# Kernel optimization log

Measured on AMD Instinct MI355X. Metric: run time of the kernel, lower is better.

## Reference

```python
import jax, jax.numpy as jnp
import numpy as np

DIM = 1024
HEADS = 16
DIM_HEAD = DIM // HEADS
SCALE = DIM_HEAD ** -0.5
LN_EPS = 1e-5


def setup_inputs() -> dict:
    key = jax.random.key(0)
    ks = jax.random.split(key, 7)
    b, n = 4, 2048
    x = jax.random.normal(ks[0], (b, n, DIM), dtype=jnp.float32)
    pos = jax.random.normal(ks[1], (b, n, DIM), dtype=jnp.float32)
    # params (torch Linear init-like scale)
    w_qkv = jax.random.normal(ks[2], (DIM, 3 * DIM), dtype=jnp.float32) * (DIM ** -0.5)
    w_out = jax.random.normal(ks[3], (DIM, DIM), dtype=jnp.float32) * (DIM ** -0.5)
    b_out = jax.random.normal(ks[4], (DIM,), dtype=jnp.float32) * 0.01
    ln_gamma = jnp.ones((DIM,), dtype=jnp.float32)
    ln_beta = jnp.zeros((DIM,), dtype=jnp.float32)
    return {"x": x, "pos": pos, "w_qkv": w_qkv, "w_out": w_out,
            "b_out": b_out, "ln_gamma": ln_gamma, "ln_beta": ln_beta}


def _layer_norm(x, gamma, beta):
    mu = jnp.mean(x, axis=-1, keepdims=True)
    var = jnp.mean(jnp.square(x - mu), axis=-1, keepdims=True)
    return (x - mu) * jax.lax.rsqrt(var + LN_EPS) * gamma + beta


def reference(x, pos, w_qkv, w_out, b_out, ln_gamma, ln_beta):
    b, n, _ = x.shape
    xn = _layer_norm(x, ln_gamma, ln_beta)
    qkv = xn @ w_qkv                                    # [b, n, 3*dim]
    q, k, v = jnp.split(qkv, 3, axis=-1)
    # [b, n, dim] -> [b, h, n, d]
    to_heads = lambda t: t.reshape(b, n, HEADS, DIM_HEAD).transpose(0, 2, 1, 3)
    q, k, v = to_heads(q), to_heads(k), to_heads(v)
    scores = jnp.einsum('bhid,bhjd->bhij', q, k) * SCALE  # [b, h, n, n]
    attn = jax.nn.softmax(scores, axis=-1)
    out = jnp.einsum('bhij,bhjd->bhid', attn, v)          # [b, h, n, d]
    out = out.transpose(0, 2, 1, 3).reshape(b, n, DIM)    # [b, n, dim]
    return (out + pos) @ w_out + b_out
```

## Files before the change

kernel.cpp:

```cpp
#include <hip/hip_runtime.h>
#include <math.h>
#include <stdint.h>

#define TOKENS 8192
#define DIM 1024
#define N3 3072
#define NSEQ 2048
#define NH 16
#define DH 64

typedef __attribute__((ext_vector_type(8))) __bf16 bf16x8;
typedef __attribute__((ext_vector_type(4))) float f32x4;
typedef __attribute__((ext_vector_type(16))) float f32x16;
typedef __attribute__((ext_vector_type(4))) short short4v;

__device__ __forceinline__ unsigned cvt2bf(float a, float b) {
    unsigned r;
    asm("v_cvt_pk_bf16_f32 %0, %1, %2" : "=v"(r) : "v"(a), "v"(b));
    return r;
}
__device__ __forceinline__ unsigned short f2bf(float f) {
    unsigned r;
    asm("v_cvt_pk_bf16_f32 %0, %1, %1" : "=v"(r) : "v"(f));
    return (unsigned short)r;
}
__device__ __forceinline__ float exp2_raw(float x) {
    float r;
    asm("v_exp_f32 %0, %1" : "=v"(r) : "v"(x));
    return r;
}
__device__ __forceinline__ float max3f(float a, float b, float c) {
    float d;
    asm("v_max3_f32 %0, %1, %2, %3" : "=v"(d) : "v"(a), "v"(b), "v"(c));
    return d;
}

__device__ __forceinline__ void glds16(const void* g, void* l) {
    __builtin_amdgcn_global_load_lds((__attribute__((address_space(1))) void*)(void*)g,
                                     (__attribute__((address_space(3))) void*)l, 16, 0, 0);
}

__global__ __launch_bounds__(256) void transpose_to_bf16(
    const float* __restrict__ in, unsigned short* __restrict__ out, int R, int C) {
    __shared__ float tile[64][65];
    int n0 = blockIdx.x * 64, k0 = blockIdx.y * 64;
    int t = threadIdx.x;
#pragma unroll
    for (int i = 0; i < 16; i++) {
        int idx = i * 256 + t;
        int r = idx >> 6, c = idx & 63;
        tile[r][c] = in[(size_t)(k0 + r) * C + n0 + c];
    }
    __syncthreads();
#pragma unroll
    for (int i = 0; i < 16; i++) {
        int idx = i * 256 + t;
        int r = idx >> 6, c = idx & 63;
        out[(size_t)(n0 + r) * R + k0 + c] = f2bf(tile[c][r]);
    }
}

__global__ __launch_bounds__(256) void ln_kernel(
    const float* __restrict__ x, const float* __restrict__ gamma,
    const float* __restrict__ beta, unsigned short* __restrict__ xn) {
    int row = blockIdx.x;
    int t = threadIdx.x;
    const float4 v = ((const float4*)(x + (size_t)row * DIM))[t];
    float s = v.x + v.y + v.z + v.w;
    float sq = v.x * v.x + v.y * v.y + v.z * v.z + v.w * v.w;
#pragma unroll
    for (int m = 1; m < 64; m <<= 1) {
        s += __shfl_xor(s, m);
        sq += __shfl_xor(sq, m);
    }
    __shared__ float ws[4], wq[4];
    int w = t >> 6, lane = t & 63;
    if (lane == 0) { ws[w] = s; wq[w] = sq; }
    __syncthreads();
    s = ws[0] + ws[1] + ws[2] + ws[3];
    sq = wq[0] + wq[1] + wq[2] + wq[3];
    float mu = s * (1.0f / DIM);
    float var = sq * (1.0f / DIM) - mu * mu;
    float rstd = rsqrtf(var + 1e-5f);
    const float4 g = ((const float4*)gamma)[t];
    const float4 bb = ((const float4*)beta)[t];
    uint2 o;
    o.x = cvt2bf((v.x - mu) * rstd * g.x + bb.x, (v.y - mu) * rstd * g.y + bb.y);
    o.y = cvt2bf((v.z - mu) * rstd * g.z + bb.z, (v.w - mu) * rstd * g.w + bb.w);
    *(uint2*)(xn + (size_t)row * DIM + t * 4) = o;
}

__device__ __forceinline__ void xcd_swizzle(int& bx, int& by) {
    int nwgx = gridDim.x;
    int nwg = nwgx * gridDim.y;
    int wg = by * nwgx + bx;
    int cpx = nwg >> 3;
    int swz = (wg & 7) * cpx + (wg >> 3);
    bx = swz % nwgx;
    by = swz / nwgx;
}

__device__ __forceinline__ void gemm_stage(
    const unsigned short* __restrict__ A, const unsigned short* __restrict__ Bt, int K,
    int brow, int bcol, int k0, char* Abuf, char* Bbuf, int w, int srow, int scol) {
#pragma unroll
    for (int i = 0; i < 2; i++) {
        int c = i * 4 + w;
        glds16(A + (size_t)(brow + 16 * c + srow) * K + k0 + scol, Abuf + c * 1024);
        glds16(Bt + (size_t)(bcol + 16 * c + srow) * K + k0 + scol, Bbuf + c * 1024);
    }
}

__device__ __forceinline__ void gemm_core(
    const unsigned short* __restrict__ A, const unsigned short* __restrict__ Bt, int K,
    int brow, int bcol, char* As, char* Bs, f32x4 acc[4][4]) {
    int t = threadIdx.x, w = t >> 6, lane = t & 63;
    int wr = w >> 1, wc = w & 1;
    int srow = lane >> 2, scol = (lane & 3) * 8;
    char* a0 = As; char* a1 = As + 8192; char* a2 = As + 16384;
    char* b0 = Bs; char* b1 = Bs + 8192; char* b2 = Bs + 16384;
    gemm_stage(A, Bt, K, brow, bcol, 0, a0, b0, w, srow, scol);
    gemm_stage(A, Bt, K, brow, bcol, 32, a1, b1, w, srow, scol);
    int NT = K >> 5;
    for (int kt = 0; kt < NT; kt++) {
        asm volatile("s_waitcnt vmcnt(4)" ::: "memory");
        __builtin_amdgcn_s_barrier();
        int kn = kt + 2; if (kn >= NT) kn -= NT;
        gemm_stage(A, Bt, K, brow, bcol, kn << 5, a2, b2, w, srow, scol);
        bf16x8 a[4], b[4];
#pragma unroll
        for (int i = 0; i < 4; i++) {
            a[i] = *(const bf16x8*)(a0 + (wr * 64 + i * 16 + (lane & 15)) * 64 + (lane >> 4) * 16);
            b[i] = *(const bf16x8*)(b0 + (wc * 64 + i * 16 + (lane & 15)) * 64 + (lane >> 4) * 16);
        }
        __builtin_amdgcn_s_setprio(1);
#pragma unroll
        for (int i = 0; i < 4; i++)
#pragma unroll
            for (int j = 0; j < 4; j++)
                acc[i][j] = __builtin_amdgcn_mfma_f32_16x16x32_bf16(a[i], b[j], acc[i][j], 0, 0, 0);
        __builtin_amdgcn_s_setprio(0);
        char* tp;
        tp = a0; a0 = a1; a1 = a2; a2 = tp;
        tp = b0; b0 = b1; b1 = b2; b2 = tp;
    }
}

#define QSCALE_LOG2E 0.18033688011112042f

__global__ __launch_bounds__(256) void gemm_qkv(
    const unsigned short* __restrict__ A, const unsigned short* __restrict__ Bt,
    unsigned short* __restrict__ Qb, unsigned short* __restrict__ Kb,
    unsigned short* __restrict__ Vt) {
    __shared__ __align__(16) char As[3 * 8192];
    __shared__ __align__(16) char Bs[3 * 8192];
    int bx = blockIdx.x, by = blockIdx.y;
    xcd_swizzle(bx, by);
    int brow = by * 128, bcol = bx * 128;
    f32x4 acc[4][4] = {};
    gemm_core(A, Bt, DIM, brow, bcol, As, Bs, acc);

    int t = threadIdx.x, w = t >> 6, lane = t & 63;
    int wr = w >> 1, wc = w & 1;
    int part = bcol >> 10;
#pragma unroll
    for (int i = 0; i < 4; i++) {
#pragma unroll
        for (int j = 0; j < 4; j++) {
            int col = bcol + wc * 64 + j * 16 + (lane & 15);
            int within = col & 1023;
            int h = within >> 6, d = within & 63;
            int rowb = brow + wr * 64 + i * 16 + (lane >> 4) * 4;
            if (part == 2) {
                int b = rowb >> 11, n = rowb & 2047;
                int bh = (b << 4) + h;
                uint2 pv;
                pv.x = cvt2bf(acc[i][j][0], acc[i][j][1]);
                pv.y = cvt2bf(acc[i][j][2], acc[i][j][3]);
                *(uint2*)(Vt + ((size_t)bh * 64 + d) * 2048 + n) = pv;
            } else {
#pragma unroll
                for (int r = 0; r < 4; r++) {
                    int row = rowb + r;
                    int b = row >> 11, n = row & 2047;
                    int bh = (b << 4) + h;
                    float val = acc[i][j][r];
                    if (part == 0)
                        Qb[((size_t)bh * 2048 + n) * 64 + d] = f2bf(val * QSCALE_LOG2E);
                    else
                        Kb[((size_t)bh * 2048 + n) * 64 + d] = f2bf(val);
                }
            }
        }
    }
}

__global__ __launch_bounds__(256) void gemm_out(
    const unsigned short* __restrict__ A, const unsigned short* __restrict__ Bt,
    const float* __restrict__ bias, float* __restrict__ out) {
    __shared__ __align__(16) char As[3 * 8192];
    __shared__ __align__(16) char Bs[3 * 8192];
    int bx = blockIdx.x, by = blockIdx.y;
    xcd_swizzle(bx, by);
    int brow = by * 128, bcol = bx * 128;
    f32x4 acc[4][4] = {};
    gemm_core(A, Bt, DIM, brow, bcol, As, Bs, acc);

    int t = threadIdx.x, w = t >> 6, lane = t & 63;
    int wr = w >> 1, wc = w & 1;
#pragma unroll
    for (int i = 0; i < 4; i++) {
#pragma unroll
        for (int j = 0; j < 4; j++) {
            int col = bcol + wc * 64 + j * 16 + (lane & 15);
            float bv = bias[col];
#pragma unroll
            for (int r = 0; r < 4; r++) {
                int row = brow + wr * 64 + i * 16 + (lane >> 4) * 4 + r;
                out[(size_t)row * DIM + col] = acc[i][j][r] + bv;
            }
        }
    }
}

#define LOG2E_THR 11.5f

__global__ __launch_bounds__(512, 4) void attn_kernel(
    const unsigned short* __restrict__ Qb, const unsigned short* __restrict__ Kb,
    const unsigned short* __restrict__ Vt, const float* __restrict__ pos,
    unsigned short* __restrict__ att) {
    __shared__ __align__(16) char Ks[4][8192];
    __shared__ __align__(16) char Vs[4][8192];
    int t = threadIdx.x, w = t >> 6, lane = t & 63;
    int l31 = lane & 31, lhi = lane >> 5;

    int L = blockIdx.y * gridDim.x + blockIdx.x;
    int bh = (L & 7) + (((L >> 3) & 7) << 3);
    int qt = L >> 6;
    int b = bh >> 4, h = bh & 15;
    int qr = qt * 256 + w * 32 + l31;

    const unsigned short* Qh = Qb + (size_t)bh * NSEQ * DH;
    const char* Khc = (const char*)(Kb + (size_t)bh * NSEQ * DH);
    const char* Vhc = (const char*)(Vt + (size_t)bh * DH * NSEQ);

    bf16x8 qf[4];
#pragma unroll
    for (int ks = 0; ks < 4; ks++)
        qf[ks] = *(const bf16x8*)(Qh + (size_t)qr * DH + ks * 16 + lhi * 8);

    f32x16 oacc[2] = {};
    float mrun = -INFINITY, lsum = 0.f;

    int ct = w >> 2, cs = w & 3;
    const char* Ksrc = Khc + (size_t)(ct * 32 + l31) * 128 + cs * 32 + lhi * 16;
    const char* Vsrc = Vhc + (size_t)(ct * 32 + l31) * 4096 + (size_t)(cs * 16 + lhi * 8) * 2;
    auto stage = [&](char* kbuf, char* vbuf, int kv0) {
        glds16(Ksrc + (size_t)kv0 * 128, kbuf + w * 1024);
        glds16(Vsrc + (size_t)kv0 * 2, vbuf + w * 1024);
    };

    auto compute = [&](const char* kc, const char* vc) {
        f32x16 st0 = {}, st1 = {};
        __builtin_amdgcn_s_setprio(1);
#pragma unroll
        for (int ks = 0; ks < 4; ks++) {
            bf16x8 kf = *(const bf16x8*)(kc + ks * 1024 + lane * 16);
            st0 = __builtin_amdgcn_mfma_f32_32x32x16_bf16(kf, qf[ks], st0, 0, 0, 0);
        }
#pragma unroll
        for (int ks = 0; ks < 4; ks++) {
            bf16x8 kf = *(const bf16x8*)(kc + (4 + ks) * 1024 + lane * 16);
            st1 = __builtin_amdgcn_mfma_f32_32x32x16_bf16(kf, qf[ks], st1, 0, 0, 0);
        }
        __builtin_amdgcn_s_setprio(0);

        float b0 = max3f(st0[0], st0[8], st1[0]);
        float b1 = max3f(st0[1], st0[9], st1[1]);
        float b2 = max3f(st0[2], st0[10], st1[2]);
        float b3 = max3f(st0[3], st0[11], st1[3]);
        float b4 = max3f(st0[4], st0[12], st1[4]);
        float b5 = max3f(st0[5], st0[13], st1[5]);
        float b6 = max3f(st0[6], st0[14], st1[6]);
        float b7 = max3f(st0[7], st0[15], st1[7]);
        float c0 = max3f(b0, b4, st1[8]);
        float c1 = max3f(b1, b5, st1[9]);
        float c2 = max3f(b2, b6, st1[10]);
        float c3 = max3f(b3, b7, st1[11]);
        float d0 = max3f(c0, c1, st1[12]);
        float d1 = max3f(c2, c3, st1[13]);
        float pm = max3f(d0, d1, fmaxf(st1[14], st1[15]));
        {
            float pa = pm, pb = pm;
            asm("v_permlane32_swap_b32 %0, %1" : "+v"(pa), "+v"(pb));
            pm = fmaxf(pa, pb);
        }
        if (!__all(pm - mrun <= LOG2E_THR)) {
            float mnew = fmaxf(mrun, pm);
            float scale = exp2_raw(mrun - mnew);
            lsum *= scale;
            oacc[0] *= scale;
            oacc[1] *= scale;
            mrun = mnew;
        }
        {
            float s0 = 0.f, s1 = 0.f, s2 = 0.f, s3 = 0.f;
#pragma unroll
            for (int r = 0; r < 16; r += 4) {
                float e0 = exp2_raw(st0[r] - mrun);
                float e1 = exp2_raw(st0[r + 1] - mrun);
                float e2 = exp2_raw(st0[r + 2] - mrun);
                float e3 = exp2_raw(st0[r + 3] - mrun);
                st0[r] = e0; st0[r + 1] = e1; st0[r + 2] = e2; st0[r + 3] = e3;
                s0 += e0; s1 += e1; s2 += e2; s3 += e3;
            }
#pragma unroll
            for (int r = 0; r < 16; r += 4) {
                float e0 = exp2_raw(st1[r] - mrun);
                float e1 = exp2_raw(st1[r + 1] - mrun);
                float e2 = exp2_raw(st1[r + 2] - mrun);
                float e3 = exp2_raw(st1[r + 3] - mrun);
                st1[r] = e0; st1[r + 1] = e1; st1[r + 2] = e2; st1[r + 3] = e3;
                s0 += e0; s1 += e1; s2 += e2; s3 += e3;
            }
            lsum += (s0 + s1) + (s2 + s3);
        }
        bf16x8 bfr[4];
#pragma unroll
        for (int ks = 0; ks < 4; ks++) {
            const f32x16& sv = (ks < 2) ? st0 : st1;
            int rb = (ks & 1) * 8;
            unsigned pa = cvt2bf(sv[rb + 0], sv[rb + 1]);
            unsigned pc = cvt2bf(sv[rb + 2], sv[rb + 3]);
            unsigned pb = cvt2bf(sv[rb + 4], sv[rb + 5]);
            unsigned pd = cvt2bf(sv[rb + 6], sv[rb + 7]);
            asm("v_permlane32_swap_b32 %0, %1" : "+v"(pa), "+v"(pb));
            asm("v_permlane32_swap_b32 %0, %1" : "+v"(pc), "+v"(pd));
            uint4 pw = {pa, pc, pb, pd};
            bfr[ks] = *(bf16x8*)&pw;
        }
        __builtin_amdgcn_s_setprio(1);
#pragma unroll
        for (int ks = 0; ks < 4; ks++)
#pragma unroll
            for (int dt = 0; dt < 2; dt++) {
                bf16x8 vf = *(const bf16x8*)(vc + (dt * 4 + ks) * 1024 + lane * 16);
                oacc[dt] = __builtin_amdgcn_mfma_f32_32x32x16_bf16(vf, bfr[ks], oacc[dt], 0, 0, 0);
            }
        __builtin_amdgcn_s_setprio(0);
    };

    char* kA0 = Ks[0]; char* kA1 = Ks[1]; char* kB0 = Ks[2]; char* kB1 = Ks[3];
    char* vA0 = Vs[0]; char* vA1 = Vs[1]; char* vB0 = Vs[2]; char* vB1 = Vs[3];
    stage(kA0, vA0, 0);
    stage(kA1, vA1, 64);

    for (int p = 0; p < 32; p += 2) {
        asm volatile("s_waitcnt vmcnt(2)" ::: "memory");
        __builtin_amdgcn_s_barrier();
        stage(kB0, vB0, ((p + 2) & 31) << 6);
        stage(kB1, vB1, ((p + 3) & 31) << 6);
        compute(kA0, vA0);
        asm volatile("s_waitcnt vmcnt(4)" ::: "memory");
        compute(kA1, vA1);
        char* tp;
        tp = kA0; kA0 = kB0; kB0 = tp;  tp = kA1; kA1 = kB1; kB1 = tp;
        tp = vA0; vA0 = vB0; vB0 = tp;  tp = vA1; vA1 = vB1; vB1 = tp;
    }

    {
        float pa = lsum, pb = lsum;
        asm("v_permlane32_swap_b32 %0, %1" : "+v"(pa), "+v"(pb));
        lsum = pa + pb;
    }
    float inv = 1.0f / lsum;
    size_t rowbase = ((size_t)b * NSEQ + qr) * DIM + h * 64;
#pragma unroll
    for (int dt = 0; dt < 2; dt++)
#pragma unroll
        for (int g4 = 0; g4 < 4; g4++) {
            int d = dt * 32 + g4 * 8 + lhi * 4;
            float4 pv = *(const float4*)(pos + rowbase + d);
            uint2 o;
            o.x = cvt2bf(oacc[dt][g4 * 4 + 0] * inv + pv.x, oacc[dt][g4 * 4 + 1] * inv + pv.y);
            o.y = cvt2bf(oacc[dt][g4 * 4 + 2] * inv + pv.z, oacc[dt][g4 * 4 + 3] * inv + pv.w);
            *(uint2*)(att + rowbase + d) = o;
        }
}

extern "C" void kernel_launch(void* const* d_in, const int* in_sizes, int n_in,
                              void* d_out, int out_size, void* d_ws, size_t ws_size,
                              hipStream_t stream) {
    const float* x = (const float*)d_in[0];
    const float* pos = (const float*)d_in[1];
    const float* w_qkv = (const float*)d_in[2];
    const float* w_out = (const float*)d_in[3];
    const float* b_out = (const float*)d_in[4];
    const float* ln_g = (const float*)d_in[5];
    const float* ln_b = (const float*)d_in[6];
    float* out = (float*)d_out;

    char* ws = (char*)d_ws;
    unsigned short* xn      = (unsigned short*)(ws);
    unsigned short* wqkv_bt = (unsigned short*)(ws + (16ull << 20));
    unsigned short* wout_bt = (unsigned short*)(ws + (22ull << 20));
    unsigned short* Qb      = (unsigned short*)(ws + (24ull << 20));
    unsigned short* Kb      = (unsigned short*)(ws + (40ull << 20));
    unsigned short* Vt      = (unsigned short*)(ws + (56ull << 20));
    unsigned short* att     = xn;

    transpose_to_bf16<<<dim3(N3 / 64, DIM / 64), 256, 0, stream>>>(w_qkv, wqkv_bt, DIM, N3);
    transpose_to_bf16<<<dim3(DIM / 64, DIM / 64), 256, 0, stream>>>(w_out, wout_bt, DIM, DIM);
    ln_kernel<<<TOKENS, 256, 0, stream>>>(x, ln_g, ln_b, xn);
    gemm_qkv<<<dim3(N3 / 128, TOKENS / 128), 256, 0, stream>>>(xn, wqkv_bt, Qb, Kb, Vt);
    attn_kernel<<<dim3(NSEQ / 256, 64), 512, 0, stream>>>(Qb, Kb, Vt, pos, att);
    gemm_out<<<dim3(DIM / 128, TOKENS / 128), 256, 0, stream>>>(att, wout_bt, b_out, out);
}
```

Baseline: 216.9 us.

## Enlarge GEMM tiles to 256x128 with 8 waves and MFMA-fragment LDS layout

Both projection GEMMs now use 512-thread blocks computing 256x128 output tiles, so each B tile is reused across twice as many rows. Shared-memory staging is rearranged so each 1 KB chunk holds a 16x32 MFMA fragment that a lane reads at a contiguous offset (lane*16), which removes per-lane strided address math and the bank conflicts that pattern could cause. The A buffers double in size, raising LDS per block, and the grid halves, which reduces the number of blocks available to fill the CUs.

```diff
diff --git a/kernel.cpp b/kernel.cpp
--- a/kernel.cpp
+++ b/kernel.cpp
@@ -100,38 +100,35 @@
     by = swz / nwgx;
 }
 
-__device__ __forceinline__ void gemm_stage(
-    const unsigned short* __restrict__ A, const unsigned short* __restrict__ Bt, int K,
-    int brow, int bcol, int k0, char* Abuf, char* Bbuf, int w, int srow, int scol) {
-#pragma unroll
-    for (int i = 0; i < 2; i++) {
-        int c = i * 4 + w;
-        glds16(A + (size_t)(brow + 16 * c + srow) * K + k0 + scol, Abuf + c * 1024);
-        glds16(Bt + (size_t)(bcol + 16 * c + srow) * K + k0 + scol, Bbuf + c * 1024);
-    }
-}
-
 __device__ __forceinline__ void gemm_core(
     const unsigned short* __restrict__ A, const unsigned short* __restrict__ Bt, int K,
     int brow, int bcol, char* As, char* Bs, f32x4 acc[4][4]) {
     int t = threadIdx.x, w = t >> 6, lane = t & 63;
-    int wr = w >> 1, wc = w & 1;
-    int srow = lane >> 2, scol = (lane & 3) * 8;
-    char* a0 = As; char* a1 = As + 8192; char* a2 = As + 16384;
+    int wm = w >> 1, wn = w & 1;
+    int r15 = lane & 15, khi = (lane >> 4) * 8;
+    const char* sA0 = (const char*)(A + (size_t)(brow + (2 * w) * 16 + r15) * K + khi);
+    const char* sA1 = (const char*)(A + (size_t)(brow + (2 * w + 1) * 16 + r15) * K + khi);
+    const char* sB  = (const char*)(Bt + (size_t)(bcol + w * 16 + r15) * K + khi);
+    char* a0 = As; char* a1 = As + 16384; char* a2 = As + 32768;
     char* b0 = Bs; char* b1 = Bs + 8192; char* b2 = Bs + 16384;
-    gemm_stage(A, Bt, K, brow, bcol, 0, a0, b0, w, srow, scol);
-    gemm_stage(A, Bt, K, brow, bcol, 32, a1, b1, w, srow, scol);
+    auto stage = [&](int k0, char* ab, char* bb) {
+        glds16(sA0 + (size_t)k0 * 2, ab + (2 * w) * 1024);
+        glds16(sA1 + (size_t)k0 * 2, ab + (2 * w + 1) * 1024);
+        glds16(sB + (size_t)k0 * 2, bb + w * 1024);
+    };
+    stage(0, a0, b0);
+    stage(32, a1, b1);
     int NT = K >> 5;
     for (int kt = 0; kt < NT; kt++) {
-        asm volatile("s_waitcnt vmcnt(4)" ::: "memory");
+        asm volatile("s_waitcnt vmcnt(3)" ::: "memory");
         __builtin_amdgcn_s_barrier();
         int kn = kt + 2; if (kn >= NT) kn -= NT;
-        gemm_stage(A, Bt, K, brow, bcol, kn << 5, a2, b2, w, srow, scol);
+        stage(kn << 5, a2, b2);
         bf16x8 a[4], b[4];
 #pragma unroll
         for (int i = 0; i < 4; i++) {
-            a[i] = *(const bf16x8*)(a0 + (wr * 64 + i * 16 + (lane & 15)) * 64 + (lane >> 4) * 16);
-            b[i] = *(const bf16x8*)(b0 + (wc * 64 + i * 16 + (lane & 15)) * 64 + (lane >> 4) * 16);
+            a[i] = *(const bf16x8*)(a0 + (wm * 4 + i) * 1024 + lane * 16);
+            b[i] = *(const bf16x8*)(b0 + (wn * 4 + i) * 1024 + lane * 16);
         }
         __builtin_amdgcn_s_setprio(1);
 #pragma unroll
@@ -148,29 +145,29 @@
 
 #define QSCALE_LOG2E 0.18033688011112042f
 
-__global__ __launch_bounds__(256) void gemm_qkv(
+__global__ __launch_bounds__(512, 4) void gemm_qkv(
     const unsigned short* __restrict__ A, const unsigned short* __restrict__ Bt,
     unsigned short* __restrict__ Qb, unsigned short* __restrict__ Kb,
     unsigned short* __restrict__ Vt) {
-    __shared__ __align__(16) char As[3 * 8192];
+    __shared__ __align__(16) char As[3 * 16384];
     __shared__ __align__(16) char Bs[3 * 8192];
     int bx = blockIdx.x, by = blockIdx.y;
     xcd_swizzle(bx, by);
-    int brow = by * 128, bcol = bx * 128;
+    int brow = by * 256, bcol = bx * 128;
     f32x4 acc[4][4] = {};
     gemm_core(A, Bt, DIM, brow, bcol, As, Bs, acc);
 
     int t = threadIdx.x, w = t >> 6, lane = t & 63;
-    int wr = w >> 1, wc = w & 1;
+    int wm = w >> 1, wn = w & 1;
     int part = bcol >> 10;
 #pragma unroll
     for (int i = 0; i < 4; i++) {
 #pragma unroll
         for (int j = 0; j < 4; j++) {
-            int col = bcol + wc * 64 + j * 16 + (lane & 15);
+            int col = bcol + wn * 64 + j * 16 + (lane & 15);
             int within = col & 1023;
             int h = within >> 6, d = within & 63;
-            int rowb = brow + wr * 64 + i * 16 + (lane >> 4) * 4;
+            int rowb = brow + wm * 64 + i * 16 + (lane >> 4) * 4;
             if (part == 2) {
                 int b = rowb >> 11, n = rowb & 2047;
                 int bh = (b << 4) + h;
@@ -195,28 +192,28 @@
     }
 }
 
-__global__ __launch_bounds__(256) void gemm_out(
+__global__ __launch_bounds__(512, 4) void gemm_out(
     const unsigned short* __restrict__ A, const unsigned short* __restrict__ Bt,
     const float* __restrict__ bias, float* __restrict__ out) {
-    __shared__ __align__(16) char As[3 * 8192];
+    __shared__ __align__(16) char As[3 * 16384];
     __shared__ __align__(16) char Bs[3 * 8192];
     int bx = blockIdx.x, by = blockIdx.y;
     xcd_swizzle(bx, by);
-    int brow = by * 128, bcol = bx * 128;
+    int brow = by * 256, bcol = bx * 128;
     f32x4 acc[4][4] = {};
     gemm_core(A, Bt, DIM, brow, bcol, As, Bs, acc);
 
     int t = threadIdx.x, w = t >> 6, lane = t & 63;
-    int wr = w >> 1, wc = w & 1;
+    int wm = w >> 1, wn = w & 1;
 #pragma unroll
     for (int i = 0; i < 4; i++) {
 #pragma unroll
         for (int j = 0; j < 4; j++) {
-            int col = bcol + wc * 64 + j * 16 + (lane & 15);
+            int col = bcol + wn * 64 + j * 16 + (lane & 15);
             float bv = bias[col];
 #pragma unroll
             for (int r = 0; r < 4; r++) {
-                int row = brow + wr * 64 + i * 16 + (lane >> 4) * 4 + r;
+                int row = brow + wm * 64 + i * 16 + (lane >> 4) * 4 + r;
                 out[(size_t)row * DIM + col] = acc[i][j][r] + bv;
             }
         }
@@ -412,7 +409,7 @@
     transpose_to_bf16<<<dim3(N3 / 64, DIM / 64), 256, 0, stream>>>(w_qkv, wqkv_bt, DIM, N3);
     transpose_to_bf16<<<dim3(DIM / 64, DIM / 64), 256, 0, stream>>>(w_out, wout_bt, DIM, DIM);
     ln_kernel<<<TOKENS, 256, 0, stream>>>(x, ln_g, ln_b, xn);
-    gemm_qkv<<<dim3(N3 / 128, TOKENS / 128), 256, 0, stream>>>(xn, wqkv_bt, Qb, Kb, Vt);
+    gemm_qkv<<<dim3(N3 / 128, TOKENS / 256), 512, 0, stream>>>(xn, wqkv_bt, Qb, Kb, Vt);
     attn_kernel<<<dim3(NSEQ / 256, 64), 512, 0, stream>>>(Qb, Kb, Vt, pos, att);
-    gemm_out<<<dim3(DIM / 128, TOKENS / 128), 256, 0, stream>>>(att, wout_bt, b_out, out);
-}
+    gemm_out<<<dim3(DIM / 128, TOKENS / 256), 512, 0, stream>>>(att, wout_bt, b_out, out);
+}
```

Result: slower. 222.7 us (+2.7%).
